# Optimization experiments

Measured on AMD Instinct MI355X. Metric: run time of the kernel, lower is better.

Reference implementation:

```python
import jax, jax.numpy as jnp
import numpy as np

N = 50000   # nodes
E = 800000  # edges (before self loops)
NEG_SLOPE = 0.2
EPS_BN = 1e-5
EPS_SM = 1e-16  # PyG softmax denominator epsilon


def gat_conv(x, src, dst, W, att_src, att_dst, bias, heads, ch):
    n = x.shape[0]
    xh = (x @ W).reshape(n, heads, ch)                       # [N,H,C]
    a_src = jnp.sum(xh * att_src, axis=-1)                   # [N,H]
    a_dst = jnp.sum(xh * att_dst, axis=-1)                   # [N,H]
    e = a_src[src] + a_dst[dst]                              # [E,H]
    e = jax.nn.leaky_relu(e, NEG_SLOPE)
    m = jax.ops.segment_max(e, dst, num_segments=n)          # segment softmax
    ex = jnp.exp(e - m[dst])
    denom = jax.ops.segment_sum(ex, dst, num_segments=n)
    alpha = ex / (denom[dst] + EPS_SM)                       # [E,H]
    msg = alpha[:, :, None] * xh[src]                        # [E,H,C]
    out = jax.ops.segment_sum(msg, dst, num_segments=n)      # [N,H,C]
    return out.reshape(n, heads * ch) + bias


def batch_norm(x, gamma, beta):
    mu = jnp.mean(x, axis=0)
    var = jnp.mean((x - mu) ** 2, axis=0)
    return (x - mu) * jax.lax.rsqrt(var + EPS_BN) * gamma + beta


def setup_inputs() -> dict:
    key = jax.random.key(0)
    ks = jax.random.split(key, 16)
    d = {}
    d['x'] = jax.random.normal(ks[0], (N, 128), jnp.float32)
    d['edge_index'] = jax.random.randint(ks[1], (2, E), 0, N, dtype=jnp.int64)
    d['W1'] = jax.random.normal(ks[2], (128, 256), jnp.float32) * 0.1
    d['as1'] = jax.random.normal(ks[3], (2, 128), jnp.float32) * 0.1
    d['ad1'] = jax.random.normal(ks[4], (2, 128), jnp.float32) * 0.1
    d['b1'] = jax.random.normal(ks[5], (256,), jnp.float32) * 0.1
    d['g1'] = jnp.ones((256,), jnp.float32)
    d['be1'] = jnp.zeros((256,), jnp.float32)
    d['W2'] = jax.random.normal(ks[6], (256, 128), jnp.float32) * 0.1
    d['as2'] = jax.random.normal(ks[7], (2, 64), jnp.float32) * 0.1
    d['ad2'] = jax.random.normal(ks[8], (2, 64), jnp.float32) * 0.1
    d['b2'] = jax.random.normal(ks[9], (128,), jnp.float32) * 0.1
    d['g2'] = jnp.ones((128,), jnp.float32)
    d['be2'] = jnp.zeros((128,), jnp.float32)
    d['W3'] = jax.random.normal(ks[10], (128, 128), jnp.float32) * 0.1
    d['as3'] = jax.random.normal(ks[11], (2, 64), jnp.float32) * 0.1
    d['ad3'] = jax.random.normal(ks[12], (2, 64), jnp.float32) * 0.1
    d['b3'] = jax.random.normal(ks[13], (128,), jnp.float32) * 0.1
    d['lw'] = jax.random.normal(ks[14], (128, 64), jnp.float32) * 0.1
    d['lb'] = jnp.zeros((64,), jnp.float32)
    return d


def reference(x, edge_index, W1, as1, ad1, b1, g1, be1,
              W2, as2, ad2, b2, g2, be2,
              W3, as3, ad3, b3, lw, lb):
    # add self loops (PyG GATConv default add_self_loops=True)
    loops = jnp.arange(N, dtype=edge_index.dtype)
    src = jnp.concatenate([edge_index[0], loops])
    dst = jnp.concatenate([edge_index[1], loops])

    h = jax.nn.relu(gat_conv(x, src, dst, W1, as1, ad1, b1, 2, 128))   # [N,256]
    h = batch_norm(h, g1, be1)
    h = jax.nn.relu(gat_conv(h, src, dst, W2, as2, ad2, b2, 2, 64))    # [N,128]
    h = batch_norm(h, g2, be2)
    h = jax.nn.relu(gat_conv(h, src, dst, W3, as3, ad3, b3, 2, 64))    # [N,128]
    return h @ lw + lb                                                 # [N,64]
```

## Files before the change

kernel.cpp:

```cpp
#include <hip/hip_runtime.h>
#include <hip/hip_bf16.h>

#define NEG_SLOPE 0.2f
#define EPS_BN 1e-5f
#define EPS_SM 1e-16f
#define CAP 128
#define DEGS 16

typedef __bf16 bf16x8 __attribute__((ext_vector_type(8)));
typedef __bf16 bf16x4 __attribute__((ext_vector_type(4)));
typedef float floatx4 __attribute__((ext_vector_type(4)));

__device__ __forceinline__ float leaky(float x) { return x > 0.f ? x : NEG_SLOPE * x; }

__global__ void k_init(const int* __restrict__ ei, int* __restrict__ flag,
                       int* __restrict__ zbase, int zwords, int e,
                       const float* __restrict__ W1, const float* __restrict__ as1,
                       const float* __restrict__ ad1, float* __restrict__ wsd) {
    if (blockIdx.x == 0) {
        __shared__ int cnt_s[256];
        int i = threadIdx.x;
        int nz = (2 * i + 1 < 2 * e && ei[2 * i + 1] != 0) ? 1 : 0;
        cnt_s[i] = nz;
        __syncthreads();
        for (int off = 128; off > 0; off >>= 1) {
            if (i < off) cnt_s[i] += cnt_s[i + off];
            __syncthreads();
        }
        if (i == 0) *flag = (cnt_s[0] < 128) ? 1 : 0;
        return;
    }
    if (blockIdx.x == 129) {
        int k = threadIdx.x;
        if (k < 128) {
            const float* wr = W1 + (size_t)k * 256;
            float s0 = 0.f, s1 = 0.f, d0 = 0.f, d1 = 0.f;
            for (int c = 0; c < 128; ++c) {
                float w0 = wr[c], w1 = wr[128 + c];
                s0 += w0 * as1[c];
                s1 += w1 * as1[128 + c];
                d0 += w0 * ad1[c];
                d1 += w1 * ad1[128 + c];
            }
            wsd[k] = s0; wsd[128 + k] = s1; wsd[256 + k] = d0; wsd[384 + k] = d1;
        }
        return;
    }
    int g = (blockIdx.x - 1) * 256 + threadIdx.x;
    const int stride = 128 * 256;
    for (int k = g; k < zwords; k += stride) zbase[k] = 0;
}

__global__ void k_hist_wconv(const int* __restrict__ ei, const int* __restrict__ flag,
                             int* __restrict__ deg, int* __restrict__ col, int e, int ebase,
                             const float* __restrict__ W1, __bf16* __restrict__ Wb1,
                             const float* __restrict__ W2, __bf16* __restrict__ Wb2,
                             const float* __restrict__ W3, __bf16* __restrict__ Wb3,
                             const float* __restrict__ x, const float* __restrict__ wsd,
                             __bf16* __restrict__ xb, float* __restrict__ asp,
                             float* __restrict__ adp, int n) {
    int g = threadIdx.x + blockIdx.x * blockDim.x;
    if (g < e) {
        bool is64 = (*flag) != 0;
        int s = is64 ? ei[2 * g] : ei[g];
        int d = is64 ? ei[2 * (e + g)] : ei[e + g];
        int r = atomicAdd(&deg[(size_t)d * DEGS], 1);
        if (r < CAP) col[((size_t)d << 7) + r] = s;
        return;
    }
    int idx = g - ebase;
    if (idx < 0) return;
    if (idx < 81920) {
        if (idx < 32768) {
            int mm = idx >> 7, kk = idx & 127;
            Wb1[idx] = (__bf16)W1[(size_t)kk * 256 + mm];
        } else if (idx < 65536) {
            int i2 = idx - 32768;
            int mm = i2 >> 8, kk = i2 & 255;
            Wb2[i2] = (__bf16)W2[(size_t)kk * 128 + mm];
        } else {
            int i3 = idx - 65536;
            int mm = i3 >> 7, kk = i3 & 127;
            Wb3[i3] = (__bf16)W3[(size_t)kk * 128 + mm];
        }
        return;
    }
    int p = idx - 81920;
    __shared__ float ws[4][128];
    for (int i = threadIdx.x; i < 512; i += 256) ws[i >> 7][i & 127] = wsd[i];
    __syncthreads();
    const int lane = threadIdx.x & 63, widx = threadIdx.x >> 6;
    const int sub = lane & 7;
    const int node = (p >> 8) * 32 + widx * 8 + (lane >> 3);
    if (node >= n) return;
    const int c0 = sub * 16;
    const float* xp = x + (size_t)node * 128 + c0;
    float xv[16];
#pragma unroll
    for (int q = 0; q < 4; ++q) {
        float4 v = *reinterpret_cast<const float4*>(xp + q * 4);
        xv[q * 4 + 0] = v.x; xv[q * 4 + 1] = v.y; xv[q * 4 + 2] = v.z; xv[q * 4 + 3] = v.w;
    }
    float s0 = 0.f, s1 = 0.f, d0 = 0.f, d1 = 0.f;
#pragma unroll
    for (int i = 0; i < 16; ++i) {
        float xi = xv[i];
        int c = c0 + i;
        s0 += xi * ws[0][c]; s1 += xi * ws[1][c];
        d0 += xi * ws[2][c]; d1 += xi * ws[3][c];
    }
#pragma unroll
    for (int off = 1; off <= 4; off <<= 1) {
        s0 += __shfl_xor(s0, off); s1 += __shfl_xor(s1, off);
        d0 += __shfl_xor(d0, off); d1 += __shfl_xor(d1, off);
    }
    bf16x8 b0, b1;
#pragma unroll
    for (int i = 0; i < 8; ++i) { b0[i] = (__bf16)xv[i]; b1[i] = (__bf16)xv[8 + i]; }
    __bf16* po = xb + (size_t)node * 128 + c0;
    *reinterpret_cast<bf16x8*>(po) = b0;
    *reinterpret_cast<bf16x8*>(po + 8) = b1;
    if (sub == 0) {
        *reinterpret_cast<float2*>(asp + 2 * node) = make_float2(s0, s1);
        *reinterpret_cast<float2*>(adp + 2 * node) = make_float2(d0, d1);
    }
}

__global__ __launch_bounds__(256) void k_agg_in(const __bf16* __restrict__ xb,
                                                const float* __restrict__ asrc,
                                                const float* __restrict__ adst,
                                                const int* __restrict__ degv,
                                                const int* __restrict__ col,
                                                __bf16* __restrict__ aggv, int n) {
    __shared__ int sA[4][80];
    __shared__ float2 sW[4][80];
    const int widx = threadIdx.x >> 6;
    const int node = blockIdx.x * 4 + widx;
    const int lane = threadIdx.x & 63;
    if (node >= n) return;
    const int t = lane & 15;
    const int g = lane >> 4;
    const int selfoff = node * 256;
    if (lane >= 48) { sA[widx][lane + 16] = selfoff; sW[widx][lane + 16] = make_float2(0.f, 0.f); }
    const char* xbt = (const char*)xb + t * 16;
    const int* crow = col + ((size_t)node << 7);
    const int deg = min(degv[(size_t)node * DEGS], CAP);
    const float2 adv = *reinterpret_cast<const float2*>(adst + 2 * node);
    const float2 asv = *reinterpret_cast<const float2*>(asrc + 2 * node);
    const float es0 = leaky(asv.x + adv.x), es1 = leaky(asv.y + adv.y);
    bf16x8 vself = *reinterpret_cast<const bf16x8*>(xbt + selfoff);
    float a0[8] = {}, a1[8] = {};
    float d0 = 0.f, d1 = 0.f;
    for (int base = 0; base < deg; base += 64) {
        const int cnt = min(64, deg - base);
        int s = (lane < cnt) ? crow[base + lane] : node;
        sA[widx][lane] = s * 256;
        float2 av = *reinterpret_cast<const float2*>(asrc + 2 * s);
        float w0 = 0.f, w1 = 0.f;
        if (lane < cnt) {
            w0 = __expf(leaky(av.x + adv.x));
            w1 = __expf(leaky(av.y + adv.y));
            d0 += w0; d1 += w1;
        }
        sW[widx][lane] = make_float2(w0, w1);
        for (int j = g; j < cnt; j += 16) {
            int o0 = sA[widx][j], o1 = sA[widx][j + 4], o2 = sA[widx][j + 8], o3 = sA[widx][j + 12];
            bf16x8 v0 = *reinterpret_cast<const bf16x8*>(xbt + o0);
            bf16x8 v1 = *reinterpret_cast<const bf16x8*>(xbt + o1);
            bf16x8 v2 = *reinterpret_cast<const bf16x8*>(xbt + o2);
            bf16x8 v3 = *reinterpret_cast<const bf16x8*>(xbt + o3);
            float2 x0 = sW[widx][j], x1 = sW[widx][j + 4], x2 = sW[widx][j + 8], x3 = sW[widx][j + 12];
#pragma unroll
            for (int q = 0; q < 8; ++q) {
                float f0 = (float)v0[q], f1 = (float)v1[q], f2 = (float)v2[q], f3 = (float)v3[q];
                a0[q] += x0.x * f0 + x1.x * f1 + x2.x * f2 + x3.x * f3;
                a1[q] += x0.y * f0 + x1.y * f1 + x2.y * f2 + x3.y * f3;
            }
        }
    }
#pragma unroll
    for (int off = 1; off <= 32; off <<= 1) {
        d0 += __shfl_xor(d0, off);
        d1 += __shfl_xor(d1, off);
    }
#pragma unroll
    for (int q = 0; q < 8; ++q) {
#pragma unroll
        for (int off = 16; off < 64; off <<= 1) {
            a0[q] += __shfl_xor(a0[q], off);
            a1[q] += __shfl_xor(a1[q], off);
        }
    }
    float exs0 = __expf(es0), exs1 = __expf(es1);
    d0 += exs0; d1 += exs1;
#pragma unroll
    for (int q = 0; q < 8; ++q) {
        a0[q] += exs0 * (float)vself[q];
        a1[q] += exs1 * (float)vself[q];
    }
    float i0 = 1.0f / (d0 + EPS_SM), i1 = 1.0f / (d1 + EPS_SM);
    if (g == 0) {
        bf16x8 st0, st1;
#pragma unroll
        for (int q = 0; q < 8; ++q) {
            st0[q] = (__bf16)(a0[q] * i0);
            st1[q] = (__bf16)(a1[q] * i1);
        }
        __bf16* po = aggv + (size_t)node * 256 + t * 8;
        *reinterpret_cast<bf16x8*>(po) = st0;
        *reinterpret_cast<bf16x8*>(po + 128) = st1;
    }
}

__global__ __launch_bounds__(256) void k_gemm_ar(const __bf16* __restrict__ A,
                                                 const __bf16* __restrict__ Bt,
                                                 const float* __restrict__ bias,
                                                 __bf16* __restrict__ Cb,
                                                 float* __restrict__ bnsums, int n) {
    __shared__ __align__(16) __bf16 As[128][72];
    __shared__ __align__(16) __bf16 Bs[128][72];
    const int row0 = blockIdx.y * 128, col0 = blockIdx.x * 128;
    const int h = col0 >> 7;
    const int lane = threadIdx.x & 63, w = threadIdx.x >> 6;
    const int m = lane & 15, quad = lane >> 4;
    floatx4 acc[2][8];
#pragma unroll
    for (int i = 0; i < 2; ++i)
#pragma unroll
        for (int j = 0; j < 8; ++j) acc[i][j] = (floatx4)0.f;
    const int sr = threadIdx.x >> 1;
    const int sk = (threadIdx.x & 1) * 32;
    for (int kc = 0; kc < 128; kc += 64) {
        {
            int grow = row0 + sr;
            if (grow < n) {
                const __bf16* p = A + (size_t)grow * 256 + h * 128 + kc + sk;
#pragma unroll
                for (int q = 0; q < 4; ++q)
                    *reinterpret_cast<bf16x8*>(&As[sr][sk + q * 8]) =
                        *reinterpret_cast<const bf16x8*>(p + q * 8);
            } else {
#pragma unroll
                for (int q = 0; q < 4; ++q)
                    *reinterpret_cast<bf16x8*>(&As[sr][sk + q * 8]) = (bf16x8)(__bf16)0.f;
            }
        }
        {
            const __bf16* p = Bt + (size_t)(col0 + sr) * 128 + kc + sk;
#pragma unroll
            for (int q = 0; q < 4; ++q)
                *reinterpret_cast<bf16x8*>(&Bs[sr][sk + q * 8]) =
                    *reinterpret_cast<const bf16x8*>(p + q * 8);
        }
        __syncthreads();
#pragma unroll
        for (int ks = 0; ks < 64; ks += 32) {
            bf16x8 a0 = *reinterpret_cast<const bf16x8*>(&As[w * 32 + m][ks + quad * 8]);
            bf16x8 a1 = *reinterpret_cast<const bf16x8*>(&As[w * 32 + 16 + m][ks + quad * 8]);
#pragma unroll
            for (int nt = 0; nt < 8; ++nt) {
                bf16x8 b = *reinterpret_cast<const bf16x8*>(&Bs[nt * 16 + m][ks + quad * 8]);
                acc[0][nt] = __builtin_amdgcn_mfma_f32_16x16x32_bf16(a0, b, acc[0][nt], 0, 0, 0);
                acc[1][nt] = __builtin_amdgcn_mfma_f32_16x16x32_bf16(a1, b, acc[1][nt], 0, 0, 0);
            }
        }
        __syncthreads();
    }
    float* redS = reinterpret_cast<float*>(As);
    float* redQ = redS + 512;
#pragma unroll
    for (int nt = 0; nt < 8; ++nt) {
        float bsv = bias[col0 + nt * 16 + m];
        float ssum = 0.f, ssq = 0.f;
#pragma unroll
        for (int mt = 0; mt < 2; ++mt)
#pragma unroll
            for (int r = 0; r < 4; ++r) {
                int row = row0 + w * 32 + mt * 16 + quad * 4 + r;
                float v = 0.f;
                if (row < n) {
                    v = fmaxf(acc[mt][nt][r] + bsv, 0.f);
                    Cb[(size_t)row * 256 + col0 + nt * 16 + m] = (__bf16)v;
                }
                ssum += v; ssq += v * v;
            }
        ssum += __shfl_xor(ssum, 16); ssum += __shfl_xor(ssum, 32);
        ssq  += __shfl_xor(ssq, 16);  ssq  += __shfl_xor(ssq, 32);
        if (quad == 0) {
            redS[w * 128 + nt * 16 + m] = ssum;
            redQ[w * 128 + nt * 16 + m] = ssq;
        }
    }
    __syncthreads();
    if (threadIdx.x < 128) {
        int c = threadIdx.x;
        float s = redS[c] + redS[128 + c] + redS[256 + c] + redS[384 + c];
        float q2 = redQ[c] + redQ[128 + c] + redQ[256 + c] + redQ[384 + c];
        atomicAdd(&bnsums[col0 + c], s);
        atomicAdd(&bnsums[256 + col0 + c], q2);
    }
}

template <int K, int LC, bool BF16IN, int NT>
__global__ __launch_bounds__(256) void k_gemm(const void* __restrict__ Ain,
                                              const __bf16* __restrict__ Bt,
                                              __bf16* __restrict__ Cb, int n, int M,
                                              const float* __restrict__ bnsums,
                                              const float* __restrict__ gam,
                                              const float* __restrict__ bet,
                                              const float* __restrict__ att_s,
                                              const float* __restrict__ att_d,
                                              float* __restrict__ asrc,
                                              float* __restrict__ adst) {
    __shared__ __align__(16) __bf16 As[128][72];
    __shared__ __align__(16) __bf16 Bs[NT * 16][72];
    __shared__ float sc_lds[K], sh_lds[K];
    const int row0 = blockIdx.y * 128, col0 = blockIdx.x * (NT * 16);
    const int lane = threadIdx.x & 63, w = threadIdx.x >> 6;
    const int m = lane & 15, quad = lane >> 4;

    if (bnsums) {
        for (int c = threadIdx.x; c < K; c += 256) {
            float mean = bnsums[c] / n;
            float var = bnsums[256 + c] / n - mean * mean;
            float sc = gam[c] * rsqrtf(var + EPS_BN);
            sc_lds[c] = sc;
            sh_lds[c] = bet[c] - mean * sc;
        }
        __syncthreads();
    }

    floatx4 acc[2][NT];
#pragma unroll
    for (int i = 0; i < 2; ++i)
#pragma unroll
        for (int j = 0; j < NT; ++j) acc[i][j] = (floatx4)0.f;

    const int sr = threadIdx.x >> 1;
    const int sk = (threadIdx.x & 1) * 32;

    for (int kc = 0; kc < K; kc += 64) {
        {
            int grow = row0 + sr;
            if (grow < n) {
                if (BF16IN) {
                    const __bf16* p = (const __bf16*)Ain + (size_t)grow * K + kc + sk;
#pragma unroll
                    for (int q = 0; q < 4; ++q) {
                        bf16x8 vv = *reinterpret_cast<const bf16x8*>(p + q * 8);
                        if (bnsums) {
                            int c = kc + sk + q * 8;
                            bf16x8 r;
#pragma unroll
                            for (int e2 = 0; e2 < 8; ++e2)
                                r[e2] = (__bf16)((float)vv[e2] * sc_lds[c + e2] + sh_lds[c + e2]);
                            vv = r;
                        }
                        *reinterpret_cast<bf16x8*>(&As[sr][sk + q * 8]) = vv;
                    }
                } else {
                    const float* p = (const float*)Ain + (size_t)grow * K + kc + sk;
#pragma unroll
                    for (int q = 0; q < 8; ++q) {
                        float4 v = *reinterpret_cast<const float4*>(p + q * 4);
                        bf16x4 cv = {(__bf16)v.x, (__bf16)v.y, (__bf16)v.z, (__bf16)v.w};
                        *reinterpret_cast<bf16x4*>(&As[sr][sk + q * 4]) = cv;
                    }
                }
            } else {
#pragma unroll
                for (int q = 0; q < 4; ++q)
                    *reinterpret_cast<bf16x8*>(&As[sr][sk + q * 8]) = (bf16x8)(__bf16)0.f;
            }
        }
        if (NT == 8) {
            const __bf16* p = Bt + (size_t)(col0 + sr) * K + kc + sk;
#pragma unroll
            for (int q = 0; q < 4; ++q)
                *reinterpret_cast<bf16x8*>(&Bs[sr][sk + q * 8]) =
                    *reinterpret_cast<const bf16x8*>(p + q * 8);
        } else {
            int sr4 = threadIdx.x >> 2, sk4 = (threadIdx.x & 3) * 16;
            const __bf16* p = Bt + (size_t)(col0 + sr4) * K + kc + sk4;
            *reinterpret_cast<bf16x8*>(&Bs[sr4][sk4]) = *reinterpret_cast<const bf16x8*>(p);
            *reinterpret_cast<bf16x8*>(&Bs[sr4][sk4 + 8]) = *reinterpret_cast<const bf16x8*>(p + 8);
        }
        __syncthreads();
#pragma unroll
        for (int ks = 0; ks < 64; ks += 32) {
            bf16x8 a0 = *reinterpret_cast<const bf16x8*>(&As[w * 32 + m][ks + quad * 8]);
            bf16x8 a1 = *reinterpret_cast<const bf16x8*>(&As[w * 32 + 16 + m][ks + quad * 8]);
#pragma unroll
            for (int nt = 0; nt < NT; ++nt) {
                bf16x8 b = *reinterpret_cast<const bf16x8*>(&Bs[nt * 16 + m][ks + quad * 8]);
                acc[0][nt] = __builtin_amdgcn_mfma_f32_16x16x32_bf16(a0, b, acc[0][nt], 0, 0, 0);
                acc[1][nt] = __builtin_amdgcn_mfma_f32_16x16x32_bf16(a1, b, acc[1][nt], 0, 0, 0);
            }
        }
        __syncthreads();
    }
#pragma unroll
    for (int mt = 0; mt < 2; ++mt)
#pragma unroll
        for (int nt = 0; nt < NT; ++nt)
#pragma unroll
            for (int r = 0; r < 4; ++r) {
                int row = row0 + w * 32 + mt * 16 + quad * 4 + r;
                if (row < n) Cb[(size_t)row * M + col0 + nt * 16 + m] = (__bf16)acc[mt][nt][r];
            }
    {
        float asv[NT], adv[NT];
#pragma unroll
        for (int nt = 0; nt < NT; ++nt) {
            int c = col0 + nt * 16 + m;
            asv[nt] = att_s[c];
            adv[nt] = att_d[c];
        }
        const int h = (col0 >> LC) & 1;
#pragma unroll
        for (int mt = 0; mt < 2; ++mt)
#pragma unroll
            for (int r = 0; r < 4; ++r) {
                int row = row0 + w * 32 + mt * 16 + quad * 4 + r;
                float pa = 0.f, pb = 0.f;
#pragma unroll
                for (int nt = 0; nt < NT; ++nt) {
                    float v = acc[mt][nt][r];
                    pa += v * asv[nt];
                    pb += v * adv[nt];
                }
#pragma unroll
                for (int off = 1; off <= 8; off <<= 1) {
                    pa += __shfl_xor(pa, off);
                    pb += __shfl_xor(pb, off);
                }
                if (m == 0 && row < n) {
                    asrc[2 * row + h] = pa;
                    adst[2 * row + h] = pb;
                }
            }
    }
}

__global__ __launch_bounds__(256) void k_lin(const float* __restrict__ A,
                                             const float* __restrict__ lw,
                                             const float* __restrict__ lb,
                                             float* __restrict__ out, int n) {
    __shared__ __align__(16) __bf16 Ahi[64][136];
    __shared__ __align__(16) __bf16 Alo[64][136];
    __shared__ __align__(16) __bf16 Bhi[64][136];
    const int row0 = blockIdx.x * 64;
    const int lane = threadIdx.x & 63, w = threadIdx.x >> 6;
    const int m = lane & 15, quad = lane >> 4;
    floatx4 acc[4];
#pragma unroll
    for (int i = 0; i < 4; ++i) acc[i] = (floatx4)0.f;
    {
        int sr = threadIdx.x >> 2, sk0 = (threadIdx.x & 3) * 32;
        int grow = row0 + sr;
#pragma unroll
        for (int q = 0; q < 8; ++q) {
            float4 v = make_float4(0.f, 0.f, 0.f, 0.f);
            if (grow < n) v = *reinterpret_cast<const float4*>(A + (size_t)grow * 128 + sk0 + q * 4);
            float vv[4] = {v.x, v.y, v.z, v.w};
#pragma unroll
            for (int i = 0; i < 4; ++i) {
                __bf16 h = (__bf16)vv[i];
                Ahi[sr][sk0 + q * 4 + i] = h;
                Alo[sr][sk0 + q * 4 + i] = (__bf16)(vv[i] - (float)h);
            }
        }
    }
    {
        int k0 = threadIdx.x >> 1, m0 = (threadIdx.x & 1) * 32;
#pragma unroll
        for (int q = 0; q < 8; ++q) {
            float4 v = *reinterpret_cast<const float4*>(lw + (size_t)k0 * 64 + m0 + q * 4);
            float vv[4] = {v.x, v.y, v.z, v.w};
#pragma unroll
            for (int i = 0; i < 4; ++i) Bhi[m0 + q * 4 + i][k0] = (__bf16)vv[i];
        }
    }
    __syncthreads();
#pragma unroll
    for (int ks = 0; ks < 128; ks += 32) {
        bf16x8 ah = *reinterpret_cast<const bf16x8*>(&Ahi[w * 16 + m][ks + quad * 8]);
        bf16x8 al = *reinterpret_cast<const bf16x8*>(&Alo[w * 16 + m][ks + quad * 8]);
#pragma unroll
        for (int nt = 0; nt < 4; ++nt) {
            bf16x8 bh = *reinterpret_cast<const bf16x8*>(&Bhi[nt * 16 + m][ks + quad * 8]);
            acc[nt] = __builtin_amdgcn_mfma_f32_16x16x32_bf16(ah, bh, acc[nt], 0, 0, 0);
            acc[nt] = __builtin_amdgcn_mfma_f32_16x16x32_bf16(al, bh, acc[nt], 0, 0, 0);
        }
    }
#pragma unroll
    for (int nt = 0; nt < 4; ++nt)
#pragma unroll
        for (int r = 0; r < 4; ++r) {
            int row = row0 + w * 16 + quad * 4 + r;
            int c = nt * 16 + m;
            if (row < n) out[(size_t)row * 64 + c] = acc[nt][r] + lb[c];
        }
}

template <int C, bool OUTBF16>
__global__ __launch_bounds__(256) void k_agg(const __bf16* __restrict__ xh,
                                             const float* __restrict__ asrc,
                                             const float* __restrict__ adst,
                                             const int* __restrict__ degv,
                                             const int* __restrict__ col,
                                             const float* __restrict__ bias,
                                             void* __restrict__ outv, int n) {
    constexpr int F = 2 * C;
    constexpr int G = F / 8;
    constexpr int NG = 64 / G;
    constexpr int GSH = (G == 32) ? 5 : 4;
    __shared__ int sA[4][80];
    __shared__ float2 sW[4][80];
    const int widx = threadIdx.x >> 6;
    const int node = blockIdx.x * 4 + widx;
    const int lane = threadIdx.x & 63;
    if (node >= n) return;
    const int t = lane & (G - 1);
    const int g = lane >> GSH;
    const bool h1 = (t * 8) >= C;
    const int selfoff = node * (F * 2);
    if (lane >= 48) { sA[widx][lane + 16] = selfoff; sW[widx][lane + 16] = make_float2(0.f, 0.f); }
    const char* xbt = (const char*)xh + t * 16;
    const int* crow = col + ((size_t)node << 7);
    const int deg = min(degv[(size_t)node * DEGS], CAP);
    const float2 adv = *reinterpret_cast<const float2*>(adst + 2 * node);
    const float2 asv = *reinterpret_cast<const float2*>(asrc + 2 * node);
    const float es0 = leaky(asv.x + adv.x), es1 = leaky(asv.y + adv.y);
    bf16x8 vself = *reinterpret_cast<const bf16x8*>(xbt + selfoff);
    float acc[8] = {};
    float d0 = 0.f, d1 = 0.f;
    for (int base = 0; base < deg; base += 64) {
        const int cnt = min(64, deg - base);
        int s = (lane < cnt) ? crow[base + lane] : node;
        sA[widx][lane] = s * (F * 2);
        float2 av = *reinterpret_cast<const float2*>(asrc + 2 * s);
        float w0 = 0.f, w1 = 0.f;
        if (lane < cnt) {
            w0 = __expf(leaky(av.x + adv.x));
            w1 = __expf(leaky(av.y + adv.y));
            d0 += w0; d1 += w1;
        }
        sW[widx][lane] = make_float2(w0, w1);
        for (int j = g; j < cnt; j += 4 * NG) {
            int o0 = sA[widx][j], o1 = sA[widx][j + NG], o2 = sA[widx][j + 2 * NG], o3 = sA[widx][j + 3 * NG];
            bf16x8 v0 = *reinterpret_cast<const bf16x8*>(xbt + o0);
            bf16x8 v1 = *reinterpret_cast<const bf16x8*>(xbt + o1);
            bf16x8 v2 = *reinterpret_cast<const bf16x8*>(xbt + o2);
            bf16x8 v3 = *reinterpret_cast<const bf16x8*>(xbt + o3);
            float2 x0 = sW[widx][j], x1 = sW[widx][j + NG], x2 = sW[widx][j + 2 * NG], x3 = sW[widx][j + 3 * NG];
            float w0 = h1 ? x0.y : x0.x;
            float w1 = h1 ? x1.y : x1.x;
            float w2 = h1 ? x2.y : x2.x;
            float w3 = h1 ? x3.y : x3.x;
#pragma unroll
            for (int q = 0; q < 8; ++q)
                acc[q] += w0 * (float)v0[q] + w1 * (float)v1[q] +
                          w2 * (float)v2[q] + w3 * (float)v3[q];
        }
    }
#pragma unroll
    for (int off = 1; off <= 32; off <<= 1) {
        d0 += __shfl_xor(d0, off);
        d1 += __shfl_xor(d1, off);
    }
#pragma unroll
    for (int q = 0; q < 8; ++q) {
#pragma unroll
        for (int off = G; off < 64; off <<= 1) acc[q] += __shfl_xor(acc[q], off);
    }
    float exs0 = __expf(es0), exs1 = __expf(es1);
    d0 += exs0; d1 += exs1;
    {
        float ws = h1 ? exs1 : exs0;
#pragma unroll
        for (int q = 0; q < 8; ++q) acc[q] += ws * (float)vself[q];
    }
    float inv = 1.0f / ((h1 ? d1 : d0) + EPS_SM);
    float o[8];
#pragma unroll
    for (int q = 0; q < 8; ++q) o[q] = fmaxf(acc[q] * inv + bias[t * 8 + q], 0.f);
    if (g == 0) {
        if constexpr (OUTBF16) {
            __bf16* po = (__bf16*)outv + (size_t)node * F + t * 8;
            bf16x8 st;
#pragma unroll
            for (int q = 0; q < 8; ++q) st[q] = (__bf16)o[q];
            *reinterpret_cast<bf16x8*>(po) = st;
        } else {
            float* po = (float*)outv + (size_t)node * F + t * 8;
            *reinterpret_cast<float4*>(po) = make_float4(o[0], o[1], o[2], o[3]);
            *reinterpret_cast<float4*>(po + 4) = make_float4(o[4], o[5], o[6], o[7]);
        }
    }
}

template <typename T>
__global__ void k_bn_stats(const T* __restrict__ x, float* __restrict__ sums,
                           float* __restrict__ sqs, int n, int f) {
    int c = threadIdx.x;
    float s = 0.f, q = 0.f;
    for (int r = blockIdx.x; r < n; r += gridDim.x) {
        float v = (float)x[(size_t)r * f + c];
        s += v; q += v * v;
    }
    atomicAdd(&sums[c], s);
    atomicAdd(&sqs[c], q);
}

extern "C" void kernel_launch(void* const* d_in, const int* in_sizes, int n_in,
                              void* d_out, int out_size, void* d_ws, size_t ws_size,
                              hipStream_t stream) {
    const float* x   = (const float*)d_in[0];
    const int*   ei  = (const int*)d_in[1];
    const float* W1  = (const float*)d_in[2];
    const float* as1 = (const float*)d_in[3];
    const float* ad1 = (const float*)d_in[4];
    const float* b1  = (const float*)d_in[5];
    const float* g1  = (const float*)d_in[6];
    const float* be1 = (const float*)d_in[7];
    const float* W2  = (const float*)d_in[8];
    const float* as2 = (const float*)d_in[9];
    const float* ad2 = (const float*)d_in[10];
    const float* b2  = (const float*)d_in[11];
    const float* g2  = (const float*)d_in[12];
    const float* be2 = (const float*)d_in[13];
    const float* W3  = (const float*)d_in[14];
    const float* as3 = (const float*)d_in[15];
    const float* ad3 = (const float*)d_in[16];
    const float* b3  = (const float*)d_in[17];
    const float* lw  = (const float*)d_in[18];
    const float* lb  = (const float*)d_in[19];
    float* outp = (float*)d_out;

    const int n = in_sizes[0] / 128;
    const int e = in_sizes[1] / 2;

    char* w = (char*)d_ws;
    size_t off = 0;
    auto alloc = [&](size_t bytes) -> void* {
        void* p = w + off;
        off += (bytes + 255) & ~(size_t)255;
        return p;
    };
    __bf16* xhb = (__bf16*)alloc((size_t)n * 256 * 2);
    __bf16* h1b = (__bf16*)alloc((size_t)n * 256 * 2);
    __bf16* h2b = (__bf16*)alloc((size_t)n * 128 * 2);
    float*  h3f = (float*)alloc((size_t)n * 128 * 4);
    int* colb   = (int*)alloc((size_t)n * CAP * 4);
    __bf16* xb  = (__bf16*)alloc((size_t)n * 128 * 2);
    __bf16* Wb1 = (__bf16*)alloc(256 * 128 * 2);
    __bf16* Wb2 = (__bf16*)alloc(128 * 256 * 2);
    __bf16* Wb3 = (__bf16*)alloc(128 * 128 * 2);
    float* wsd  = (float*)alloc(512 * 4);
    int* flag   = (int*)alloc(256);
    float* as1p = (float*)alloc((size_t)n * 2 * 4);
    float* ad1p = (float*)alloc((size_t)n * 2 * 4);
    float* as2p = (float*)alloc((size_t)n * 2 * 4);
    float* ad2p = (float*)alloc((size_t)n * 2 * 4);
    float* as3p = (float*)alloc((size_t)n * 2 * 4);
    float* ad3p = (float*)alloc((size_t)n * 2 * 4);
    char* zb_begin = (char*)(w + off);
    int* deg    = (int*)alloc((size_t)n * DEGS * 4);
    float* bn1  = (float*)alloc(512 * 4);
    float* bn2  = (float*)alloc(512 * 4);
    char* zb_end = (char*)(w + off);
    const int zwords = (int)((zb_end - zb_begin) / 4);

    k_init<<<130, 256, 0, stream>>>(ei, flag, (int*)zb_begin, zwords, e, W1, as1, ad1, wsd);

    const int ebase = ((e + 255) / 256) * 256;
    const int preblocks = (n + 31) / 32;
    const int histblocks = ebase / 256 + 320 + preblocks;
    k_hist_wconv<<<histblocks, 256, 0, stream>>>(ei, flag, deg, colb, e, ebase,
                                                 W1, Wb1, W2, Wb2, W3, Wb3,
                                                 x, wsd, xb, as1p, ad1p, n);

    const int nwb = (n + 3) / 4;
    const int nrow = (n + 127) / 128;

    k_agg_in<<<nwb, 256, 0, stream>>>(xb, as1p, ad1p, deg, colb, xhb, n);
    k_gemm_ar<<<dim3(2, nrow), 256, 0, stream>>>(xhb, Wb1, b1, h1b, bn1, n);

    k_gemm<256, 6, true, 4><<<dim3(2, nrow), 256, 0, stream>>>(
        h1b, Wb2, xhb, n, 128, bn1, g1, be1, as2, ad2, as2p, ad2p);
    k_agg<64, true><<<nwb, 256, 0, stream>>>(xhb, as2p, ad2p, deg, colb, b2, h2b, n);
    k_bn_stats<__bf16><<<256, 128, 0, stream>>>(h2b, bn2, bn2 + 256, n, 128);

    k_gemm<128, 6, true, 4><<<dim3(2, nrow), 256, 0, stream>>>(
        h2b, Wb3, xhb, n, 128, bn2, g2, be2, as3, ad3, as3p, ad3p);
    k_agg<64, false><<<nwb, 256, 0, stream>>>(xhb, as3p, ad3p, deg, colb, b3, h3f, n);

    k_lin<<<(n + 63) / 64, 256, 0, stream>>>(h3f, lw, lb, outp, n);
}
```

Measured before the change: 433.7 us.

## Fuse final GAT aggregation with output linear layer

Replaces the separate layer-3 aggregation kernel and the MFMA-based final linear kernel with one kernel. Each wavefront aggregates one node, writes the ReLU'd row to shared memory, then computes the 64 outputs with scalar FMAs against a bf16 copy of lw held in LDS. This drops the fp32 h3 intermediate write/read and one launch. In exchange each block now loads 16KB of weights into LDS, which may cut occupancy, and the linear layer uses scalar math with bf16 weights instead of split-precision MFMA. The bf16 copy of lw is produced in the preprocessing kernel.

```diff
diff --git a/kernel.cpp b/kernel.cpp
--- a/kernel.cpp
+++ b/kernel.cpp
@@ -56,6 +56,7 @@
                              const float* __restrict__ W1, __bf16* __restrict__ Wb1,
                              const float* __restrict__ W2, __bf16* __restrict__ Wb2,
                              const float* __restrict__ W3, __bf16* __restrict__ Wb3,
+                             const float* __restrict__ lw, __bf16* __restrict__ lwb,
                              const float* __restrict__ x, const float* __restrict__ wsd,
                              __bf16* __restrict__ xb, float* __restrict__ asp,
                              float* __restrict__ adp, int n) {
@@ -70,7 +71,7 @@
     }
     int idx = g - ebase;
     if (idx < 0) return;
-    if (idx < 81920) {
+    if (idx < 90112) {
         if (idx < 32768) {
             int mm = idx >> 7, kk = idx & 127;
             Wb1[idx] = (__bf16)W1[(size_t)kk * 256 + mm];
@@ -78,14 +79,17 @@
             int i2 = idx - 32768;
             int mm = i2 >> 8, kk = i2 & 255;
             Wb2[i2] = (__bf16)W2[(size_t)kk * 128 + mm];
-        } else {
+        } else if (idx < 81920) {
             int i3 = idx - 65536;
             int mm = i3 >> 7, kk = i3 & 127;
             Wb3[i3] = (__bf16)W3[(size_t)kk * 128 + mm];
+        } else {
+            int i4 = idx - 81920;
+            lwb[i4] = (__bf16)lw[i4];
         }
         return;
     }
-    int p = idx - 81920;
+    int p = idx - 90112;
     __shared__ float ws[4][128];
     for (int i = threadIdx.x; i < 512; i += 256) ws[i >> 7][i & 127] = wsd[i];
     __syncthreads();
@@ -440,67 +444,6 @@
                 }
             }
     }
-}
-
-__global__ __launch_bounds__(256) void k_lin(const float* __restrict__ A,
-                                             const float* __restrict__ lw,
-                                             const float* __restrict__ lb,
-                                             float* __restrict__ out, int n) {
-    __shared__ __align__(16) __bf16 Ahi[64][136];
-    __shared__ __align__(16) __bf16 Alo[64][136];
-    __shared__ __align__(16) __bf16 Bhi[64][136];
-    const int row0 = blockIdx.x * 64;
-    const int lane = threadIdx.x & 63, w = threadIdx.x >> 6;
-    const int m = lane & 15, quad = lane >> 4;
-    floatx4 acc[4];
-#pragma unroll
-    for (int i = 0; i < 4; ++i) acc[i] = (floatx4)0.f;
-    {
-        int sr = threadIdx.x >> 2, sk0 = (threadIdx.x & 3) * 32;
-        int grow = row0 + sr;
-#pragma unroll
-        for (int q = 0; q < 8; ++q) {
-            float4 v = make_float4(0.f, 0.f, 0.f, 0.f);
-            if (grow < n) v = *reinterpret_cast<const float4*>(A + (size_t)grow * 128 + sk0 + q * 4);
-            float vv[4] = {v.x, v.y, v.z, v.w};
-#pragma unroll
-            for (int i = 0; i < 4; ++i) {
-                __bf16 h = (__bf16)vv[i];
-                Ahi[sr][sk0 + q * 4 + i] = h;
-                Alo[sr][sk0 + q * 4 + i] = (__bf16)(vv[i] - (float)h);
-            }
-        }
-    }
-    {
-        int k0 = threadIdx.x >> 1, m0 = (threadIdx.x & 1) * 32;
-#pragma unroll
-        for (int q = 0; q < 8; ++q) {
-            float4 v = *reinterpret_cast<const float4*>(lw + (size_t)k0 * 64 + m0 + q * 4);
-            float vv[4] = {v.x, v.y, v.z, v.w};
-#pragma unroll
-            for (int i = 0; i < 4; ++i) Bhi[m0 + q * 4 + i][k0] = (__bf16)vv[i];
-        }
-    }
-    __syncthreads();
-#pragma unroll
-    for (int ks = 0; ks < 128; ks += 32) {
-        bf16x8 ah = *reinterpret_cast<const bf16x8*>(&Ahi[w * 16 + m][ks + quad * 8]);
-        bf16x8 al = *reinterpret_cast<const bf16x8*>(&Alo[w * 16 + m][ks + quad * 8]);
-#pragma unroll
-        for (int nt = 0; nt < 4; ++nt) {
-            bf16x8 bh = *reinterpret_cast<const bf16x8*>(&Bhi[nt * 16 + m][ks + quad * 8]);
-            acc[nt] = __builtin_amdgcn_mfma_f32_16x16x32_bf16(ah, bh, acc[nt], 0, 0, 0);
-            acc[nt] = __builtin_amdgcn_mfma_f32_16x16x32_bf16(al, bh, acc[nt], 0, 0, 0);
-        }
-    }
-#pragma unroll
-    for (int nt = 0; nt < 4; ++nt)
-#pragma unroll
-        for (int r = 0; r < 4; ++r) {
-            int row = row0 + w * 16 + quad * 4 + r;
-            int c = nt * 16 + m;
-            if (row < n) out[(size_t)row * 64 + c] = acc[nt][r] + lb[c];
-        }
 }
 
 template <int C, bool OUTBF16>
@@ -600,6 +543,101 @@
     }
 }
 
+__global__ __launch_bounds__(256) void k_agg_lin(const __bf16* __restrict__ xh,
+                                                 const float* __restrict__ asrc,
+                                                 const float* __restrict__ adst,
+                                                 const int* __restrict__ degv,
+                                                 const int* __restrict__ col,
+                                                 const float* __restrict__ bias,
+                                                 const __bf16* __restrict__ lwb,
+                                                 const float* __restrict__ lb,
+                                                 float* __restrict__ out, int n) {
+    constexpr int C = 64, F = 128, G = 16;
+    __shared__ int sA[4][80];
+    __shared__ float2 sW[4][80];
+    __shared__ __align__(16) __bf16 lwL[128 * 64];
+    __shared__ float orow[4][128];
+    for (int i = threadIdx.x; i < 4096; i += 256)
+        reinterpret_cast<int*>(lwL)[i] = reinterpret_cast<const int*>(lwb)[i];
+    __syncthreads();
+    const int widx = threadIdx.x >> 6;
+    const int node = blockIdx.x * 4 + widx;
+    const int lane = threadIdx.x & 63;
+    if (node >= n) return;
+    const int t = lane & (G - 1);
+    const int g = lane >> 4;
+    const bool h1 = (t * 8) >= C;
+    const int selfoff = node * (F * 2);
+    if (lane >= 48) { sA[widx][lane + 16] = selfoff; sW[widx][lane + 16] = make_float2(0.f, 0.f); }
+    const char* xbt = (const char*)xh + t * 16;
+    const int* crow = col + ((size_t)node << 7);
+    const int deg = min(degv[(size_t)node * DEGS], CAP);
+    const float2 adv = *reinterpret_cast<const float2*>(adst + 2 * node);
+    const float2 asv = *reinterpret_cast<const float2*>(asrc + 2 * node);
+    const float es0 = leaky(asv.x + adv.x), es1 = leaky(asv.y + adv.y);
+    bf16x8 vself = *reinterpret_cast<const bf16x8*>(xbt + selfoff);
+    float acc[8] = {};
+    float d0 = 0.f, d1 = 0.f;
+    for (int base = 0; base < deg; base += 64) {
+        const int cnt = min(64, deg - base);
+        int s = (lane < cnt) ? crow[base + lane] : node;
+        sA[widx][lane] = s * (F * 2);
+        float2 av = *reinterpret_cast<const float2*>(asrc + 2 * s);
+        float w0 = 0.f, w1 = 0.f;
+        if (lane < cnt) {
+            w0 = __expf(leaky(av.x + adv.x));
+            w1 = __expf(leaky(av.y + adv.y));
+            d0 += w0; d1 += w1;
+        }
+        sW[widx][lane] = make_float2(w0, w1);
+        for (int j = g; j < cnt; j += 16) {
+            int o0 = sA[widx][j], o1 = sA[widx][j + 4], o2 = sA[widx][j + 8], o3 = sA[widx][j + 12];
+            bf16x8 v0 = *reinterpret_cast<const bf16x8*>(xbt + o0);
+            bf16x8 v1 = *reinterpret_cast<const bf16x8*>(xbt + o1);
+            bf16x8 v2 = *reinterpret_cast<const bf16x8*>(xbt + o2);
+            bf16x8 v3 = *reinterpret_cast<const bf16x8*>(xbt + o3);
+            float2 x0 = sW[widx][j], x1 = sW[widx][j + 4], x2 = sW[widx][j + 8], x3 = sW[widx][j + 12];
+            float w0 = h1 ? x0.y : x0.x;
+            float w1 = h1 ? x1.y : x1.x;
+            float w2 = h1 ? x2.y : x2.x;
+            float w3 = h1 ? x3.y : x3.x;
+#pragma unroll
+            for (int q = 0; q < 8; ++q)
+                acc[q] += w0 * (float)v0[q] + w1 * (float)v1[q] +
+                          w2 * (float)v2[q] + w3 * (float)v3[q];
+        }
+    }
+#pragma unroll
+    for (int off = 1; off <= 32; off <<= 1) {
+        d0 += __shfl_xor(d0, off);
+        d1 += __shfl_xor(d1, off);
+    }
+#pragma unroll
+    for (int q = 0; q < 8; ++q) {
+#pragma unroll
+        for (int off = G; off < 64; off <<= 1) acc[q] += __shfl_xor(acc[q], off);
+    }
+    float exs0 = __expf(es0), exs1 = __expf(es1);
+    d0 += exs0; d1 += exs1;
+    {
+        float ws = h1 ? exs1 : exs0;
+#pragma unroll
+        for (int q = 0; q < 8; ++q) acc[q] += ws * (float)vself[q];
+    }
+    float inv = 1.0f / ((h1 ? d1 : d0) + EPS_SM);
+    if (g == 0) {
+#pragma unroll
+        for (int q = 0; q < 8; ++q)
+            orow[widx][t * 8 + q] = fmaxf(acc[q] * inv + bias[t * 8 + q], 0.f);
+    }
+    const int c = lane;
+    float a2 = lb[c];
+#pragma unroll 8
+    for (int k = 0; k < 128; ++k)
+        a2 += orow[widx][k] * (float)lwL[k * 64 + c];
+    out[(size_t)node * 64 + c] = a2;
+}
+
 template <typename T>
 __global__ void k_bn_stats(const T* __restrict__ x, float* __restrict__ sums,
                            float* __restrict__ sqs, int n, int f) {
@@ -651,12 +689,12 @@
     __bf16* xhb = (__bf16*)alloc((size_t)n * 256 * 2);
     __bf16* h1b = (__bf16*)alloc((size_t)n * 256 * 2);
     __bf16* h2b = (__bf16*)alloc((size_t)n * 128 * 2);
-    float*  h3f = (float*)alloc((size_t)n * 128 * 4);
     int* colb   = (int*)alloc((size_t)n * CAP * 4);
     __bf16* xb  = (__bf16*)alloc((size_t)n * 128 * 2);
     __bf16* Wb1 = (__bf16*)alloc(256 * 128 * 2);
     __bf16* Wb2 = (__bf16*)alloc(128 * 256 * 2);
     __bf16* Wb3 = (__bf16*)alloc(128 * 128 * 2);
+    __bf16* lwb = (__bf16*)alloc(128 * 64 * 2);
     float* wsd  = (float*)alloc(512 * 4);
     int* flag   = (int*)alloc(256);
     float* as1p = (float*)alloc((size_t)n * 2 * 4);
@@ -676,10 +714,10 @@
 
     const int ebase = ((e + 255) / 256) * 256;
     const int preblocks = (n + 31) / 32;
-    const int histblocks = ebase / 256 + 320 + preblocks;
+    const int histblocks = ebase / 256 + 352 + preblocks;
     k_hist_wconv<<<histblocks, 256, 0, stream>>>(ei, flag, deg, colb, e, ebase,
                                                  W1, Wb1, W2, Wb2, W3, Wb3,
-                                                 x, wsd, xb, as1p, ad1p, n);
+                                                 lw, lwb, x, wsd, xb, as1p, ad1p, n);
 
     const int nwb = (n + 3) / 4;
     const int nrow = (n + 127) / 128;
@@ -694,7 +732,5 @@
 
     k_gemm<128, 6, true, 4><<<dim3(2, nrow), 256, 0, stream>>>(
         h2b, Wb3, xhb, n, 128, bn2, g2, be2, as3, ad3, as3p, ad3p);
-    k_agg<64, false><<<nwb, 256, 0, stream>>>(xhb, as3p, ad3p, deg, colb, b3, h3f, n);
-
-    k_lin<<<(n + 63) / 64, 256, 0, stream>>>(h3f, lw, lb, outp, n);
-}
+    k_agg_lin<<<nwb, 256, 0, stream>>>(xhb, as3p, ad3p, deg, colb, b3, lwb, lb, outp, n);
+}
```

Measured after the change: 450.0 us. 3.8% more time.
